# Kernel tuning notes

Hardware: AMD Instinct MI355X
Metric: run time of the kernel (lower is better)

Reference implementation:

```python
import jax, jax.numpy as jnp
import numpy as np

B, C, H, W = 8, 192, 128, 128
CQK = C // 3  # 64


def setup_inputs() -> dict:
    key = jax.random.key(0)
    ks = jax.random.split(key, 8)
    s = 0.05
    return {
        "x": jax.random.normal(ks[0], (B, C, H, W), dtype=jnp.float32),
        "Wq": jax.random.normal(ks[1], (CQK, C), dtype=jnp.float32) * s,
        "bq": jax.random.normal(ks[2], (CQK,), dtype=jnp.float32) * s,
        "Wk": jax.random.normal(ks[3], (CQK, C), dtype=jnp.float32) * s,
        "bk": jax.random.normal(ks[4], (CQK,), dtype=jnp.float32) * s,
        "Wv": jax.random.normal(ks[5], (C, C), dtype=jnp.float32) * s,
        "bv": jax.random.normal(ks[6], (C,), dtype=jnp.float32) * s,
        "gamma": jnp.zeros((1,), dtype=jnp.float32),
    }


def _conv1x1(x, Wt, b):
    # x: [B,C,H,W], Wt: [Cout,Cin] -> [B,Cout,H,W]
    return jnp.einsum('bchw,oc->bohw', x, Wt) + b[None, :, None, None]


def reference(x, Wq, bq, Wk, bk, Wv, bv, gamma):
    Q = _conv1x1(x, Wq, bq)  # [B,CQK,H,W]
    K = _conv1x1(x, Wk, bk)  # [B,CQK,H,W]
    V = _conv1x1(x, Wv, bv)  # [B,C,H,W]

    # Column (vertical) attention logits: query at (h,w) attends to (h2,w)
    e_h = jnp.einsum('bchw,bcgw->bhwg', Q, K)  # [B,H,W,H]
    # mask diagonal h==h2 with -inf (as in MaskAttention)
    diag = jnp.where(jnp.eye(H, dtype=bool), -jnp.inf, 0.0).astype(x.dtype)
    e_h = e_h + diag[:, None, :]  # broadcast over B and W

    # Row (horizontal) attention logits: query at (h,w) attends to (h,w2)
    e_w = jnp.einsum('bchw,bchv->bhwv', Q, K)  # [B,H,W,W]

    # joint softmax over concatenated H+W axis
    att = jax.nn.softmax(jnp.concatenate([e_h, e_w], axis=3), axis=3)
    att_h = att[:, :, :, :H]      # [B,H,W,H]
    att_w = att[:, :, :, H:]      # [B,H,W,W]

    out_h = jnp.einsum('bhwg,bcgw->bchw', att_h, V)
    out_w = jnp.einsum('bhwv,bchv->bchw', att_w, V)
    return gamma * (out_h + out_w) + x
```

## Files before the change

kernel.cpp:

```cpp
#include <hip/hip_runtime.h>
#include <math.h>


#define B_   8
#define C_   192
#define CQK_ 64
#define H_   128
#define W_   128
#define HW_  (H_*W_)

typedef unsigned short u16;
typedef __attribute__((ext_vector_type(8))) short    s16x8;
typedef __attribute__((ext_vector_type(4))) float    f32x4;
typedef __attribute__((ext_vector_type(2))) unsigned u32x2;
#define MFMA_BF16 __builtin_amdgcn_mfma_f32_16x16x32_bf16

__device__ __forceinline__ u16 f2b(float f) {
    unsigned u = __float_as_uint(f);
    return (u16)((u + 0x7fffu + ((u >> 16) & 1u)) >> 16);
}
__device__ __forceinline__ float b2f(u16 v) {
    return __uint_as_float(((unsigned)v) << 16);
}
__device__ __forceinline__ void gll16(const u16* gsrc, unsigned lds_byte) {
    asm volatile("s_mov_b32 m0, %1\n\t"
                 "global_load_lds_dwordx4 %0, off"
                 :: "v"(gsrc), "s"(lds_byte) : "memory");
}

__global__ __launch_bounds__(256) void kwcast(
    const float* __restrict__ Wq, const float* __restrict__ bq,
    const float* __restrict__ Wk, const float* __restrict__ bk,
    const float* __restrict__ Wv, const float* __restrict__ bv,
    u16* __restrict__ Wb, float* __restrict__ Bb)
{
    const int o = blockIdx.x;
    const float *row, *bias; int oo;
    if (o < 64)        { row = Wq; bias = bq; oo = o;       }
    else if (o < 128)  { row = Wk; bias = bk; oo = o - 64;  }
    else               { row = Wv; bias = bv; oo = o - 128; }
    const int t = threadIdx.x;
    if (t < C_) {
        const int p = t >> 6, cc = t & 63;
        Wb[p*20480 + o*64 + (((cc >> 3) ^ (o & 7)) << 3) + (cc & 7)]
            = f2b(row[oo*C_ + t]);
    }
    if (t == C_) Bb[o] = bias[oo];
}

__global__ __launch_bounds__(256) void kxt(
    const float* __restrict__ x, u16* __restrict__ xT)
{
    __shared__ u16 T[24576];
    const int h = blockIdx.x, b = blockIdx.y;
    const float* xb = x + (size_t)b*C_*HW_ + h*W_;
    const int t = threadIdx.x;
    #pragma unroll
    for (int i = 0; i < 24; ++i) {
        const int ridx = i*256 + t;
        const int c = ridx >> 5, wq = (ridx & 31) << 2;
        const f32x4 v = *(const f32x4*)(const void*)(xb + (size_t)c*HW_ + wq);
        u32x2 pk;
        pk.x = (unsigned)f2b(v[0]) | ((unsigned)f2b(v[1]) << 16);
        pk.y = (unsigned)f2b(v[2]) | ((unsigned)f2b(v[3]) << 16);
        *(u32x2*)(void*)&T[c*128 + (((wq >> 3) ^ ((c >> 3) & 15)) << 3) + (wq & 7)] = pk;
    }
    __syncthreads();
    u16* dst = xT + (size_t)(b*H_ + h)*24576;
    #pragma unroll
    for (int i = 0; i < 12; ++i) {
        const int oidx = i*256 + t;
        const int p = oidx >> 10, w = (oidx >> 3) & 127, cp = oidx & 7;
        s16x8 pk;
        #pragma unroll
        for (int e = 0; e < 8; ++e) {
            const int c = p*64 + ((cp ^ (w & 7)) << 3) + e;
            pk[e] = (short)T[c*128 + ((((w >> 3)) ^ ((c >> 3) & 15)) << 3) + (w & 7)];
        }
        *(s16x8*)(void*)(dst + p*8192 + w*64 + cp*8) = pk;
    }
}

__global__ __launch_bounds__(256, 2) void kprojM(
    const u16* __restrict__ xT,
    const u16* __restrict__ Wb, const float* __restrict__ Bb,
    u16* __restrict__ Qc, u16* __restrict__ Kc, u16* __restrict__ Vn)
{
    __shared__ u16 lds[36864];
    u16* ldsW = lds + 16384;
    u16* ldsV = lds + 8192;
    const int h = blockIdx.x, b = blockIdx.y;
    const int t = threadIdx.x, lane = t & 63, wid = t >> 6;
    const int l15 = lane & 15, q = lane >> 4;

    f32x4 acc[8][5];
    #pragma unroll
    for (int ct = 0; ct < 5; ++ct) {
        const float bv = Bb[(ct*4 + wid)*16 + l15];
        #pragma unroll
        for (int r = 0; r < 8; ++r) acc[r][ct] = (f32x4){bv, bv, bv, bv};
    }

    const u16* xTb = xT + (size_t)(b*H_ + h)*24576;
    const unsigned wofs = __builtin_amdgcn_readfirstlane(32768u + (unsigned)wid*1024u);
    const unsigned aofs = __builtin_amdgcn_readfirstlane((unsigned)wid*1024u);

#define STAGE_W(p) do {                                                   \
    const u16* g = Wb + (p)*20480 + wid*512 + lane*8;                     \
    _Pragma("unroll")                                                     \
    for (int i = 0; i < 10; ++i) gll16(g + i*2048, wofs + i*4096); } while(0)
#define STAGE_A(p, ab) do {                                               \
    const u16* g = xTb + (p)*8192 + wid*512 + lane*8;                     \
    _Pragma("unroll")                                                     \
    for (int i = 0; i < 4; ++i)                                           \
        gll16(g + i*2048, aofs + (ab)*16384u + i*4096); } while(0)
#define MFMA_PHASE(ab) do {                                               \
    const u16* bA = lds + (ab)*8192;                                      \
    __builtin_amdgcn_s_setprio(1);                                        \
    _Pragma("unroll")                                                     \
    for (int ks = 0; ks < 2; ++ks) {                                      \
        s16x8 bf[5];                                                      \
        _Pragma("unroll")                                                 \
        for (int ct = 0; ct < 5; ++ct) {                                  \
            const int o = (ct*4 + wid)*16 + l15;                          \
            bf[ct] = *(const s16x8*)(const void*)                         \
                     &ldsW[o*64 + (((ks*4 + q) ^ (o & 7)) << 3)];         \
        }                                                                 \
        _Pragma("unroll")                                                 \
        for (int r = 0; r < 8; ++r) {                                     \
            const int w = r*16 + l15;                                     \
            const s16x8 af = *(const s16x8*)(const void*)                 \
                     &bA[w*64 + (((ks*4 + q) ^ (w & 7)) << 3)];           \
            _Pragma("unroll")                                             \
            for (int ct = 0; ct < 5; ++ct)                                \
                acc[r][ct] = MFMA_BF16(af, bf[ct], acc[r][ct], 0, 0, 0);  \
        }                                                                 \
    }                                                                     \
    __builtin_amdgcn_s_setprio(0); } while(0)

    STAGE_W(0); STAGE_A(0, 0); STAGE_A(1, 1);
    asm volatile("s_waitcnt vmcnt(4)" ::: "memory");
    __builtin_amdgcn_s_barrier();
    MFMA_PHASE(0);
    asm volatile("s_waitcnt lgkmcnt(0)" ::: "memory");
    __builtin_amdgcn_s_barrier();
    STAGE_W(1); STAGE_A(2, 0);
    asm volatile("s_waitcnt vmcnt(4)" ::: "memory");
    __builtin_amdgcn_s_barrier();
    MFMA_PHASE(1);
    asm volatile("s_waitcnt lgkmcnt(0)" ::: "memory");
    __builtin_amdgcn_s_barrier();
    STAGE_W(2);
    asm volatile("s_waitcnt vmcnt(0)" ::: "memory");
    __builtin_amdgcn_s_barrier();
    MFMA_PHASE(0);
    asm volatile("s_waitcnt lgkmcnt(0)" ::: "memory");
    __builtin_amdgcn_s_barrier();

    {
        const int oc = wid*16 + l15;
        #pragma unroll
        for (int r = 0; r < 8; ++r)
            #pragma unroll
            for (int rg = 0; rg < 4; ++rg) {
                const int w = r*16 + q*4 + rg;
                const size_t base = ((size_t)(b*W_ + w)*H_ + h)*CQK_ + oc;
                Qc[base] = f2b(acc[r][0][rg]);
                Kc[base] = f2b(acc[r][1][rg]);
            }
    }
    #pragma unroll
    for (int ct = 2; ct < 5; ++ct) {
        const int c = (ct - 2)*64 + wid*16 + l15;
        #pragma unroll
        for (int r = 0; r < 8; ++r) {
            const int w0 = r*16 + q*4;
            u32x2 pk;
            pk.x = (unsigned)f2b(acc[r][ct][0]) | ((unsigned)f2b(acc[r][ct][1]) << 16);
            pk.y = (unsigned)f2b(acc[r][ct][2]) | ((unsigned)f2b(acc[r][ct][3]) << 16);
            *(u32x2*)(void*)&ldsV[c*128 + (((w0 >> 3) ^ (c & 7)) << 3) + (w0 & 7)] = pk;
        }
    }
    asm volatile("s_waitcnt lgkmcnt(0)" ::: "memory");
    __builtin_amdgcn_s_barrier();
    #pragma unroll
    for (int i = 0; i < 12; ++i) {
        const int idx = i*256 + t;
        const int c = idx >> 4, j = idx & 15;
        const s16x8 v = *(const s16x8*)(const void*)&ldsV[c*128 + j*8];
        *(s16x8*)(void*)&Vn[(size_t)(b*C_ + c)*HW_ + h*W_ + ((j ^ (c & 7)) << 3)] = v;
    }
#undef STAGE_W
#undef STAGE_A
#undef MFMA_PHASE
}

__global__ __launch_bounds__(256) void ktrv(
    const u16* __restrict__ Vn, u16* __restrict__ Vc)
{
    __shared__ u16 T[128*128];
    const int c = blockIdx.x, b = blockIdx.y;
    const u16* src = Vn + (size_t)(b*C_ + c)*HW_;
    u16*       dst = Vc + (size_t)(b*C_ + c)*HW_;
    const int t = threadIdx.x;
    for (int idx = t; idx < 128*16; idx += 256) {
        const int hh = idx >> 4, o = idx & 15;
        s16x8 v = *(const s16x8*)(void*)(src + hh*128 + o*8);
        *(s16x8*)(void*)(T + hh*128 + ((o ^ (hh & 7)) << 3)) = v;
    }
    __syncthreads();
    const int w = t & 127, half = t >> 7;
    for (int seg = 0; seg < 8; ++seg) {
        const int h0 = half*64 + seg*8;
        s16x8 pk;
        #pragma unroll
        for (int k = 0; k < 8; ++k) {
            const int hh = h0 + k;
            const int chunk = (w >> 3) ^ (hh & 7);
            pk[k] = (short)T[hh*128 + (chunk << 3) + (w & 7)];
        }
        *(s16x8*)(void*)(dst + w*128 + h0) = pk;
    }
}

__global__ __launch_bounds__(512) void kC(
    const u16* __restrict__ Qc, const u16* __restrict__ Kc,
    const u16* __restrict__ Vc,
    u16* __restrict__ O2, float* __restrict__ Mh, float* __restrict__ Sh)
{
    extern __shared__ char smem[];
    char* ldsQ = smem;
    char* ldsK = smem + 16384;
    char* ldsP = smem;
    char* ldsV = smem + 32768;
    const int w = blockIdx.x, b = blockIdx.y;
    const int t = threadIdx.x, lane = t & 63, wid = t >> 6;
    const int l15 = lane & 15, q = lane >> 4;

    {
        const u16* qs = Qc + (size_t)(b*W_ + w)*H_*CQK_;
        const u16* ks = Kc + (size_t)(b*W_ + w)*H_*CQK_;
        for (int idx = t; idx < 1024; idx += 512) {
            const int r = idx >> 3, o = idx & 7, so = ((o ^ (r & 7)) << 4);
            *(s16x8*)(ldsQ + r*128 + so) = *(const s16x8*)(void*)(qs + idx*8);
            *(s16x8*)(ldsK + r*128 + so) = *(const s16x8*)(void*)(ks + idx*8);
        }
        for (int idx = t; idx < 3072; idx += 512) {
            const int c = idx >> 4, o = idx & 15;
            s16x8 v = *(const s16x8*)(void*)
                      (Vc + ((size_t)(b*C_ + c)*W_ + w)*H_ + o*8);
            *(s16x8*)(ldsV + c*256 + ((o ^ (c & 7)) << 4)) = v;
        }
    }
    __syncthreads();

    f32x4 accS[8];
    #pragma unroll
    for (int i = 0; i < 8; ++i) accS[i] = (f32x4){0.f,0.f,0.f,0.f};
    const int arow = (wid << 4) + l15;
    #pragma unroll
    for (int ks = 0; ks < 2; ++ks) {
        const int ch = ks*4 + q;
        s16x8 af = *(const s16x8*)(ldsQ + arow*128 + ((ch ^ (arow & 7)) << 4));
        #pragma unroll
        for (int gt = 0; gt < 8; ++gt) {
            const int br = (gt << 4) + l15;
            s16x8 bf = *(const s16x8*)(ldsK + br*128 + ((ch ^ (br & 7)) << 4));
            accS[gt] = MFMA_BF16(af, bf, accS[gt], 0, 0, 0);
        }
    }
    __syncthreads();

    #pragma unroll
    for (int r = 0; r < 4; ++r) {
        const int hh = (wid << 4) + (q << 2) + r;
        #pragma unroll
        for (int gt = 0; gt < 8; ++gt)
            if ((gt << 4) + l15 == hh) accS[gt][r] = -3.0e38f;
        float m = -3.0e38f;
        #pragma unroll
        for (int gt = 0; gt < 8; ++gt) m = fmaxf(m, accS[gt][r]);
        m = fmaxf(m, __shfl_xor(m, 1)); m = fmaxf(m, __shfl_xor(m, 2));
        m = fmaxf(m, __shfl_xor(m, 4)); m = fmaxf(m, __shfl_xor(m, 8));
        float s = 0.f;
        #pragma unroll
        for (int gt = 0; gt < 8; ++gt) {
            const float e = __expf(accS[gt][r] - m);
            s += e;
            const int g = (gt << 4) + l15;
            *(u16*)(ldsP + hh*256 + (((g >> 3) ^ (hh & 7)) << 4) + (g & 7)*2)
                = f2b(e);
        }
        s += __shfl_xor(s, 1); s += __shfl_xor(s, 2);
        s += __shfl_xor(s, 4); s += __shfl_xor(s, 8);
        if (l15 == 0) {
            Mh[(b*W_ + w)*H_ + hh] = m;
            Sh[(b*W_ + w)*H_ + hh] = s;
        }
    }
    __syncthreads();

    f32x4 accO[12];
    #pragma unroll
    for (int i = 0; i < 12; ++i) accO[i] = (f32x4){0.f,0.f,0.f,0.f};
    #pragma unroll
    for (int ks = 0; ks < 4; ++ks) {
        const int ch = ks*4 + q;
        const int pr = (wid << 4) + l15;
        s16x8 af = *(const s16x8*)(ldsP + pr*256 + ((ch ^ (pr & 7)) << 4));
        #pragma unroll
        for (int ct = 0; ct < 12; ++ct) {
            const int vr = (ct << 4) + l15;
            s16x8 bf = *(const s16x8*)(ldsV + vr*256 + ((ch ^ (vr & 7)) << 4));
            accO[ct] = MFMA_BF16(af, bf, accO[ct], 0, 0, 0);
        }
    }
    #pragma unroll
    for (int ct = 0; ct < 12; ++ct) {
        const int c = (ct << 4) + l15;
        #pragma unroll
        for (int r = 0; r < 4; ++r) {
            const int hh = (wid << 4) + (q << 2) + r;
            O2[((size_t)(b*W_ + w)*H_ + hh)*C_ + c] = f2b(accO[ct][r]);
        }
    }
}

__global__ __launch_bounds__(512) void kR(
    const u16* __restrict__ Qc, const u16* __restrict__ Kc,
    const u16* __restrict__ Vn, const u16* __restrict__ O2,
    const float* __restrict__ Mh, const float* __restrict__ Sh,
    const float* __restrict__ x, const float* __restrict__ gamma,
    float* __restrict__ out)
{
    extern __shared__ char smem[];
    char*  ldsQ  = smem;
    char*  ldsK  = smem + 16384;
    char*  ldsP  = smem;
    char*  ldsV  = smem + 32768;
    char*  ldsO2 = smem + 81920;
    float* sMh = (float*)(smem + 133120);
    float* sSh = sMh + 128;
    float* sMw = sSh + 128;
    float* sSw = sMw + 128;
    const int h = blockIdx.x, b = blockIdx.y;
    const int t = threadIdx.x, lane = t & 63, wid = t >> 6;
    const int l15 = lane & 15, q = lane >> 4;
    const float gam = gamma[0];

    for (int idx = t; idx < 1024; idx += 512) {
        const int r = idx >> 3, o = idx & 7, so = ((o ^ (r & 7)) << 4);
        const size_t g = ((size_t)(b*W_ + r)*H_ + h)*CQK_ + o*8;
        *(s16x8*)(ldsQ + r*128 + so) = *(const s16x8*)(void*)(Qc + g);
        *(s16x8*)(ldsK + r*128 + so) = *(const s16x8*)(void*)(Kc + g);
    }
    for (int idx = t; idx < 3072; idx += 512) {
        const int c = idx >> 4, o = idx & 15;
        s16x8 v = *(const s16x8*)(void*)
                  (Vn + (size_t)(b*C_ + c)*HW_ + h*W_ + o*8);
        *(s16x8*)(ldsV + c*256 + ((o ^ (c & 7)) << 4)) = v;
    }
    for (int idx = t; idx < 3200; idx += 512) {
        const int r = idx / 25, o = idx - r*25;
        if (o < 24) {
            s16x8 v = *(const s16x8*)(void*)
                      (O2 + ((size_t)(b*W_ + r)*H_ + h)*C_ + o*8);
            *(s16x8*)(ldsO2 + r*400 + o*16) = v;
        }
    }
    if (t < 128) {
        sMh[t] = Mh[(b*W_ + t)*H_ + h];
        sSh[t] = Sh[(b*W_ + t)*H_ + h];
    }
    __syncthreads();

    f32x4 accS[8];
    #pragma unroll
    for (int i = 0; i < 8; ++i) accS[i] = (f32x4){0.f,0.f,0.f,0.f};
    const int arow = (wid << 4) + l15;
    #pragma unroll
    for (int ks = 0; ks < 2; ++ks) {
        const int ch = ks*4 + q;
        s16x8 af = *(const s16x8*)(ldsQ + arow*128 + ((ch ^ (arow & 7)) << 4));
        #pragma unroll
        for (int vt = 0; vt < 8; ++vt) {
            const int br = (vt << 4) + l15;
            s16x8 bf = *(const s16x8*)(ldsK + br*128 + ((ch ^ (br & 7)) << 4));
            accS[vt] = MFMA_BF16(af, bf, accS[vt], 0, 0, 0);
        }
    }
    __syncthreads();

    #pragma unroll
    for (int r = 0; r < 4; ++r) {
        const int ww = (wid << 4) + (q << 2) + r;
        float m = -3.0e38f;
        #pragma unroll
        for (int vt = 0; vt < 8; ++vt) m = fmaxf(m, accS[vt][r]);
        m = fmaxf(m, __shfl_xor(m, 1)); m = fmaxf(m, __shfl_xor(m, 2));
        m = fmaxf(m, __shfl_xor(m, 4)); m = fmaxf(m, __shfl_xor(m, 8));
        float s = 0.f;
        #pragma unroll
        for (int vt = 0; vt < 8; ++vt) {
            const float e = __expf(accS[vt][r] - m);
            s += e;
            const int v = (vt << 4) + l15;
            *(u16*)(ldsP + ww*256 + (((v >> 3) ^ (ww & 7)) << 4) + (v & 7)*2)
                = f2b(e);
        }
        s += __shfl_xor(s, 1); s += __shfl_xor(s, 2);
        s += __shfl_xor(s, 4); s += __shfl_xor(s, 8);
        if (l15 == 0) { sMw[ww] = m; sSw[ww] = s; }
    }
    __syncthreads();

    f32x4 accO[12];
    #pragma unroll
    for (int i = 0; i < 12; ++i) accO[i] = (f32x4){0.f,0.f,0.f,0.f};
    const int prow = (wid << 4) + l15;
    #pragma unroll
    for (int ks = 0; ks < 4; ++ks) {
        const int ch = ks*4 + q;
        s16x8 bfp = *(const s16x8*)(ldsP + prow*256 + ((ch ^ (prow & 7)) << 4));
        #pragma unroll
        for (int ct = 0; ct < 12; ++ct) {
            const int vr = (ct << 4) + l15;
            s16x8 afv = *(const s16x8*)(ldsV + vr*256 + ((ch ^ (vr & 7)) << 4));
            accO[ct] = MFMA_BF16(afv, bfp, accO[ct], 0, 0, 0);
        }
    }

    const int ww = (wid << 4) + l15;
    const float mh = sMh[ww], shv = sSh[ww];
    const float mw = sMw[ww], swv = sSw[ww];
    const float M  = fmaxf(mh, mw);
    const float S  = shv*__expf(mh - M) + swv*__expf(mw - M);
    const float scw = __expf(mw - M) / S;
    const float sch = __expf(mh - M) / S;
    const size_t gb = (size_t)b*C_*HW_ + h*W_ + ww;
    #pragma unroll
    for (int ct = 0; ct < 12; ++ct) {
        #pragma unroll
        for (int r = 0; r < 4; ++r) {
            const int c = (ct << 4) + (q << 2) + r;
            const float o2 = b2f(*(const u16*)(ldsO2 + ww*400 + c*2));
            const size_t ga = gb + (size_t)c*HW_;
            out[ga] = gam*(accO[ct][r]*scw + o2*sch) + x[ga];
        }
    }
}

extern "C" void kernel_launch(void* const* d_in, const int* in_sizes, int n_in,
                              void* d_out, int out_size, void* d_ws, size_t ws_size,
                              hipStream_t stream)
{
    const float* x  = (const float*)d_in[0];
    const float* Wq = (const float*)d_in[1];
    const float* bq = (const float*)d_in[2];
    const float* Wk = (const float*)d_in[3];
    const float* bk = (const float*)d_in[4];
    const float* Wv = (const float*)d_in[5];
    const float* bv = (const float*)d_in[6];
    const float* gm = (const float*)d_in[7];
    float* out = (float*)d_out;

    u16* Qc = (u16*)d_ws;
    u16* Kc = Qc + 8388608;
    u16* Vn = Kc + 8388608;
    u16* Vc = Vn + 25165824;
    u16* O2 = Vc + 25165824;
    u16* xT = O2;
    float* Mh = (float*)(O2 + 25165824);
    float* Sh = Mh + 131072;
    u16*  Wb = (u16*)(Sh + 131072);
    float* Bb = (float*)(Wb + 61440);

    hipLaunchKernelGGL(kwcast, dim3(320), dim3(256), 0, stream,
                       Wq, bq, Wk, bk, Wv, bv, Wb, Bb);
    hipLaunchKernelGGL(kxt, dim3(H_, B_), dim3(256), 0, stream, x, xT);
    hipLaunchKernelGGL(kprojM, dim3(H_, B_), dim3(256), 0, stream,
                       xT, Wb, Bb, Qc, Kc, Vn);
    hipLaunchKernelGGL(ktrv, dim3(C_, B_), dim3(256), 0, stream, Vn, Vc);
    hipLaunchKernelGGL(kC, dim3(W_, B_), dim3(512), 81920, stream,
                       Qc, Kc, Vc, O2, Mh, Sh);
    hipLaunchKernelGGL(kR, dim3(H_, B_), dim3(512), 135168, stream,
                       Qc, Kc, Vn, O2, Mh, Sh, x, gm, out);
}
```

Baseline: 204.1 us.

## Split row-attention V product into two channel halves to shrink LDS footprint

```diff
diff --git a/kernel.cpp b/kernel.cpp
--- a/kernel.cpp
+++ b/kernel.cpp
@@ -321,12 +321,12 @@
         #pragma unroll
         for (int r = 0; r < 4; ++r) {
             const int hh = (wid << 4) + (q << 2) + r;
-            O2[((size_t)(b*W_ + w)*H_ + hh)*C_ + c] = f2b(accO[ct][r]);
-        }
-    }
-}
-
-__global__ __launch_bounds__(512) void kR(
+            O2[((size_t)(b*H_ + hh)*W_ + w)*C_ + c] = f2b(accO[ct][r]);
+        }
+    }
+}
+
+__global__ __launch_bounds__(512, 4) void kR(
     const u16* __restrict__ Qc, const u16* __restrict__ Kc,
     const u16* __restrict__ Vn, const u16* __restrict__ O2,
     const float* __restrict__ Mh, const float* __restrict__ Sh,
@@ -334,12 +334,11 @@
     float* __restrict__ out)
 {
     extern __shared__ char smem[];
-    char*  ldsQ  = smem;
-    char*  ldsK  = smem + 16384;
-    char*  ldsP  = smem;
-    char*  ldsV  = smem + 32768;
-    char*  ldsO2 = smem + 81920;
-    float* sMh = (float*)(smem + 133120);
+    char*  ldsQ = smem;
+    char*  ldsK = smem + 16384;
+    char*  ldsP = smem;
+    char*  ldsV = smem + 32768;
+    float* sMh = (float*)(smem + 57344);
     float* sSh = sMh + 128;
     float* sMw = sSh + 128;
     float* sSw = sMw + 128;
@@ -348,25 +347,24 @@
     const int l15 = lane & 15, q = lane >> 4;
     const float gam = gamma[0];
 
+    s16x8 vh2[3];
+    #pragma unroll
+    for (int i = 0; i < 3; ++i) {
+        const int idx = i*512 + t;
+        const int c = 96 + (idx >> 4), o = idx & 15;
+        vh2[i] = *(const s16x8*)(void*)(Vn + (size_t)(b*C_ + c)*HW_ + h*W_ + o*8);
+    }
     for (int idx = t; idx < 1024; idx += 512) {
         const int r = idx >> 3, o = idx & 7, so = ((o ^ (r & 7)) << 4);
         const size_t g = ((size_t)(b*W_ + r)*H_ + h)*CQK_ + o*8;
         *(s16x8*)(ldsQ + r*128 + so) = *(const s16x8*)(void*)(Qc + g);
         *(s16x8*)(ldsK + r*128 + so) = *(const s16x8*)(void*)(Kc + g);
     }
-    for (int idx = t; idx < 3072; idx += 512) {
+    for (int idx = t; idx < 1536; idx += 512) {
         const int c = idx >> 4, o = idx & 15;
         s16x8 v = *(const s16x8*)(void*)
                   (Vn + (size_t)(b*C_ + c)*HW_ + h*W_ + o*8);
         *(s16x8*)(ldsV + c*256 + ((o ^ (c & 7)) << 4)) = v;
-    }
-    for (int idx = t; idx < 3200; idx += 512) {
-        const int r = idx / 25, o = idx - r*25;
-        if (o < 24) {
-            s16x8 v = *(const s16x8*)(void*)
-                      (O2 + ((size_t)(b*W_ + r)*H_ + h)*C_ + o*8);
-            *(s16x8*)(ldsO2 + r*400 + o*16) = v;
-        }
     }
     if (t < 128) {
         sMh[t] = Mh[(b*W_ + t)*H_ + h];
@@ -414,20 +412,28 @@
     }
     __syncthreads();
 
-    f32x4 accO[12];
-    #pragma unroll
-    for (int i = 0; i < 12; ++i) accO[i] = (f32x4){0.f,0.f,0.f,0.f};
     const int prow = (wid << 4) + l15;
+    f32x4 accO[6];
+    #pragma unroll
+    for (int i = 0; i < 6; ++i) accO[i] = (f32x4){0.f,0.f,0.f,0.f};
     #pragma unroll
     for (int ks = 0; ks < 4; ++ks) {
         const int ch = ks*4 + q;
         s16x8 bfp = *(const s16x8*)(ldsP + prow*256 + ((ch ^ (prow & 7)) << 4));
         #pragma unroll
-        for (int ct = 0; ct < 12; ++ct) {
+        for (int ct = 0; ct < 6; ++ct) {
             const int vr = (ct << 4) + l15;
             s16x8 afv = *(const s16x8*)(ldsV + vr*256 + ((ch ^ (vr & 7)) << 4));
             accO[ct] = MFMA_BF16(afv, bfp, accO[ct], 0, 0, 0);
         }
+    }
+    __syncthreads();
+
+    #pragma unroll
+    for (int i = 0; i < 3; ++i) {
+        const int idx = i*512 + t;
+        const int lc = idx >> 4, o = idx & 15;
+        *(s16x8*)(ldsV + lc*256 + ((o ^ ((lc + 96) & 7)) << 4)) = vh2[i];
     }
 
     const int ww = (wid << 4) + l15;
@@ -437,15 +443,43 @@
     const float S  = shv*__expf(mh - M) + swv*__expf(mw - M);
     const float scw = __expf(mw - M) / S;
     const float sch = __expf(mh - M) / S;
+    const u16* o2p = O2 + ((size_t)(b*H_ + h)*W_ + ww)*C_;
     const size_t gb = (size_t)b*C_*HW_ + h*W_ + ww;
-    #pragma unroll
-    for (int ct = 0; ct < 12; ++ct) {
+
+    #pragma unroll
+    for (int ct = 0; ct < 6; ++ct) {
         #pragma unroll
         for (int r = 0; r < 4; ++r) {
-            const int c = (ct << 4) + (q << 2) + r;
-            const float o2 = b2f(*(const u16*)(ldsO2 + ww*400 + c*2));
+            const int c = ct*16 + q*4 + r;
+            const float o2 = b2f(o2p[c]);
             const size_t ga = gb + (size_t)c*HW_;
             out[ga] = gam*(accO[ct][r]*scw + o2*sch) + x[ga];
+        }
+    }
+    __syncthreads();
+
+    f32x4 accO2[6];
+    #pragma unroll
+    for (int i = 0; i < 6; ++i) accO2[i] = (f32x4){0.f,0.f,0.f,0.f};
+    #pragma unroll
+    for (int ks = 0; ks < 4; ++ks) {
+        const int ch = ks*4 + q;
+        s16x8 bfp = *(const s16x8*)(ldsP + prow*256 + ((ch ^ (prow & 7)) << 4));
+        #pragma unroll
+        for (int ct = 0; ct < 6; ++ct) {
+            const int lr = (ct << 4) + l15;
+            s16x8 afv = *(const s16x8*)(ldsV + lr*256 + ((ch ^ ((lr + 96) & 7)) << 4));
+            accO2[ct] = MFMA_BF16(afv, bfp, accO2[ct], 0, 0, 0);
+        }
+    }
+    #pragma unroll
+    for (int ct = 0; ct < 6; ++ct) {
+        #pragma unroll
+        for (int r = 0; r < 4; ++r) {
+            const int c = 96 + ct*16 + q*4 + r;
+            const float o2 = b2f(o2p[c]);
+            const size_t ga = gb + (size_t)c*HW_;
+            out[ga] = gam*(accO2[ct][r]*scw + o2*sch) + x[ga];
         }
     }
 }
@@ -483,6 +517,6 @@
     hipLaunchKernelGGL(ktrv, dim3(C_, B_), dim3(256), 0, stream, Vn, Vc);
     hipLaunchKernelGGL(kC, dim3(W_, B_), dim3(512), 81920, stream,
                        Qc, Kc, Vc, O2, Mh, Sh);
-    hipLaunchKernelGGL(kR, dim3(H_, B_), dim3(512), 135168, stream,
+    hipLaunchKernelGGL(kR, dim3(H_, B_), dim3(512), 59392, stream,
                        Qc, Kc, Vn, O2, Mh, Sh, x, gm, out);
 }
```

Result: slower. 219.8 us (+7.7%).

## Shrink LDS in attention kernels by staging V in chunks and register-resident Q

Applied to the files above, without the earlier changes.

```diff
diff --git a/kernel.cpp b/kernel.cpp
--- a/kernel.cpp
+++ b/kernel.cpp
@@ -223,45 +223,54 @@
     }
 }
 
-__global__ __launch_bounds__(512) void kC(
+__global__ __launch_bounds__(512, 6) void kC(
     const u16* __restrict__ Qc, const u16* __restrict__ Kc,
     const u16* __restrict__ Vc,
     u16* __restrict__ O2, float* __restrict__ Mh, float* __restrict__ Sh)
 {
     extern __shared__ char smem[];
-    char* ldsQ = smem;
-    char* ldsK = smem + 16384;
+    char* ldsK = smem;
     char* ldsP = smem;
     char* ldsV = smem + 32768;
     const int w = blockIdx.x, b = blockIdx.y;
     const int t = threadIdx.x, lane = t & 63, wid = t >> 6;
     const int l15 = lane & 15, q = lane >> 4;
-
+    const int arow = (wid << 4) + l15;
+
+    const u16* qrow = Qc + ((size_t)(b*W_ + w)*H_ + arow)*CQK_;
+    s16x8 qf0 = *(const s16x8*)(const void*)(qrow + q*8);
+    s16x8 qf1 = *(const s16x8*)(const void*)(qrow + (4 + q)*8);
+    s16x8 vh[2];
+    #pragma unroll
+    for (int i = 0; i < 2; ++i) {
+        const int idx = i*512 + t;
+        const int c = 64 + (idx >> 4), o = idx & 15;
+        vh[i] = *(const s16x8*)(const void*)
+                (Vc + ((size_t)(b*C_ + c)*W_ + w)*H_ + o*8);
+    }
     {
-        const u16* qs = Qc + (size_t)(b*W_ + w)*H_*CQK_;
-        const u16* ks = Kc + (size_t)(b*W_ + w)*H_*CQK_;
+        const u16* ksrc = Kc + (size_t)(b*W_ + w)*H_*CQK_;
         for (int idx = t; idx < 1024; idx += 512) {
-            const int r = idx >> 3, o = idx & 7, so = ((o ^ (r & 7)) << 4);
-            *(s16x8*)(ldsQ + r*128 + so) = *(const s16x8*)(void*)(qs + idx*8);
-            *(s16x8*)(ldsK + r*128 + so) = *(const s16x8*)(void*)(ks + idx*8);
-        }
-        for (int idx = t; idx < 3072; idx += 512) {
-            const int c = idx >> 4, o = idx & 15;
-            s16x8 v = *(const s16x8*)(void*)
-                      (Vc + ((size_t)(b*C_ + c)*W_ + w)*H_ + o*8);
-            *(s16x8*)(ldsV + c*256 + ((o ^ (c & 7)) << 4)) = v;
-        }
+            const int r = idx >> 3, o = idx & 7;
+            *(s16x8*)(ldsK + r*128 + ((o ^ (r & 7)) << 4)) =
+                *(const s16x8*)(const void*)(ksrc + idx*8);
+        }
+    }
+    for (int idx = t; idx < 1024; idx += 512) {
+        const int lc = idx >> 4, o = idx & 15;
+        *(s16x8*)(ldsV + lc*256 + ((o ^ (lc & 7)) << 4)) =
+            *(const s16x8*)(const void*)
+            (Vc + ((size_t)(b*C_ + lc)*W_ + w)*H_ + o*8);
     }
     __syncthreads();
 
     f32x4 accS[8];
     #pragma unroll
     for (int i = 0; i < 8; ++i) accS[i] = (f32x4){0.f,0.f,0.f,0.f};
-    const int arow = (wid << 4) + l15;
     #pragma unroll
     for (int ks = 0; ks < 2; ++ks) {
         const int ch = ks*4 + q;
-        s16x8 af = *(const s16x8*)(ldsQ + arow*128 + ((ch ^ (arow & 7)) << 4));
+        const s16x8 af = ks ? qf1 : qf0;
         #pragma unroll
         for (int gt = 0; gt < 8; ++gt) {
             const int br = (gt << 4) + l15;
@@ -298,35 +307,71 @@
             Sh[(b*W_ + w)*H_ + hh] = s;
         }
     }
-    __syncthreads();
-
-    f32x4 accO[12];
-    #pragma unroll
-    for (int i = 0; i < 12; ++i) accO[i] = (f32x4){0.f,0.f,0.f,0.f};
-    #pragma unroll
-    for (int ks = 0; ks < 4; ++ks) {
-        const int ch = ks*4 + q;
-        const int pr = (wid << 4) + l15;
-        s16x8 af = *(const s16x8*)(ldsP + pr*256 + ((ch ^ (pr & 7)) << 4));
-        #pragma unroll
-        for (int ct = 0; ct < 12; ++ct) {
-            const int vr = (ct << 4) + l15;
-            s16x8 bf = *(const s16x8*)(ldsV + vr*256 + ((ch ^ (vr & 7)) << 4));
-            accO[ct] = MFMA_BF16(af, bf, accO[ct], 0, 0, 0);
-        }
-    }
-    #pragma unroll
-    for (int ct = 0; ct < 12; ++ct) {
-        const int c = (ct << 4) + l15;
-        #pragma unroll
-        for (int r = 0; r < 4; ++r) {
-            const int hh = (wid << 4) + (q << 2) + r;
-            O2[((size_t)(b*W_ + w)*H_ + hh)*C_ + c] = f2b(accO[ct][r]);
-        }
-    }
-}
-
-__global__ __launch_bounds__(512) void kR(
+
+#define KC_PV(accv) do {                                                  \
+    _Pragma("unroll")                                                     \
+    for (int ks = 0; ks < 4; ++ks) {                                      \
+        const int ch = ks*4 + q;                                          \
+        s16x8 afp = *(const s16x8*)(ldsP + arow*256 + ((ch ^ (arow & 7)) << 4)); \
+        _Pragma("unroll")                                                 \
+        for (int ct = 0; ct < 4; ++ct) {                                  \
+            const int vr = (ct << 4) + l15;                               \
+            s16x8 bfv = *(const s16x8*)(ldsV + vr*256 + ((ch ^ (vr & 7)) << 4)); \
+            accv[ct] = MFMA_BF16(afp, bfv, accv[ct], 0, 0, 0);            \
+        }                                                                 \
+    } } while(0)
+#define KC_O2W(accv, cb) do {                                             \
+    _Pragma("unroll")                                                     \
+    for (int ct = 0; ct < 4; ++ct) {                                      \
+        const int c = (cb) + (ct << 4) + l15;                             \
+        _Pragma("unroll")                                                 \
+        for (int r = 0; r < 4; ++r) {                                     \
+            const int hh = (wid << 4) + (q << 2) + r;                     \
+            O2[((size_t)(b*H_ + hh)*W_ + w)*C_ + c] = f2b(accv[ct][r]);   \
+        }                                                                 \
+    } } while(0)
+
+    f32x4 accO[4];
+    #pragma unroll
+    for (int i = 0; i < 4; ++i) accO[i] = (f32x4){0.f,0.f,0.f,0.f};
+    KC_PV(accO);
+    __syncthreads();
+    #pragma unroll
+    for (int i = 0; i < 2; ++i) {
+        const int idx = i*512 + t;
+        const int lc = idx >> 4, o = idx & 15;
+        *(s16x8*)(ldsV + lc*256 + ((o ^ (lc & 7)) << 4)) = vh[i];
+    }
+    #pragma unroll
+    for (int i = 0; i < 2; ++i) {
+        const int idx = i*512 + t;
+        const int c = 128 + (idx >> 4), o = idx & 15;
+        vh[i] = *(const s16x8*)(const void*)
+                (Vc + ((size_t)(b*C_ + c)*W_ + w)*H_ + o*8);
+    }
+    __syncthreads();
+    KC_O2W(accO, 0);
+    #pragma unroll
+    for (int i = 0; i < 4; ++i) accO[i] = (f32x4){0.f,0.f,0.f,0.f};
+    KC_PV(accO);
+    __syncthreads();
+    #pragma unroll
+    for (int i = 0; i < 2; ++i) {
+        const int idx = i*512 + t;
+        const int lc = idx >> 4, o = idx & 15;
+        *(s16x8*)(ldsV + lc*256 + ((o ^ (lc & 7)) << 4)) = vh[i];
+    }
+    __syncthreads();
+    KC_O2W(accO, 64);
+    #pragma unroll
+    for (int i = 0; i < 4; ++i) accO[i] = (f32x4){0.f,0.f,0.f,0.f};
+    KC_PV(accO);
+    KC_O2W(accO, 128);
+#undef KC_PV
+#undef KC_O2W
+}
+
+__global__ __launch_bounds__(512, 6) void kR(
     const u16* __restrict__ Qc, const u16* __restrict__ Kc,
     const u16* __restrict__ Vn, const u16* __restrict__ O2,
     const float* __restrict__ Mh, const float* __restrict__ Sh,
@@ -334,54 +379,50 @@
     float* __restrict__ out)
 {
     extern __shared__ char smem[];
-    char*  ldsQ  = smem;
-    char*  ldsK  = smem + 16384;
+    char*  ldsK  = smem;
     char*  ldsP  = smem;
     char*  ldsV  = smem + 32768;
-    char*  ldsO2 = smem + 81920;
-    float* sMh = (float*)(smem + 133120);
-    float* sSh = sMh + 128;
-    float* sMw = sSh + 128;
-    float* sSw = sMw + 128;
+    float* sScw  = (float*)(smem + 49152);
+    float* sSch  = (float*)(smem + 49664);
     const int h = blockIdx.x, b = blockIdx.y;
     const int t = threadIdx.x, lane = t & 63, wid = t >> 6;
     const int l15 = lane & 15, q = lane >> 4;
+    const int arow = (wid << 4) + l15;
+    const int wbase = (wid << 4) + (q << 2);
     const float gam = gamma[0];
 
+    const u16* qrow = Qc + ((size_t)(b*W_ + arow)*H_ + h)*CQK_;
+    s16x8 qf0 = *(const s16x8*)(const void*)(qrow + q*8);
+    s16x8 qf1 = *(const s16x8*)(const void*)(qrow + (4 + q)*8);
+    s16x8 vh[2];
+    #pragma unroll
+    for (int i = 0; i < 2; ++i) {
+        const int idx = i*512 + t;
+        const int c = 64 + (idx >> 4), o = idx & 15;
+        vh[i] = *(const s16x8*)(const void*)
+                (Vn + (size_t)(b*C_ + c)*HW_ + h*W_ + o*8);
+    }
     for (int idx = t; idx < 1024; idx += 512) {
-        const int r = idx >> 3, o = idx & 7, so = ((o ^ (r & 7)) << 4);
-        const size_t g = ((size_t)(b*W_ + r)*H_ + h)*CQK_ + o*8;
-        *(s16x8*)(ldsQ + r*128 + so) = *(const s16x8*)(void*)(Qc + g);
-        *(s16x8*)(ldsK + r*128 + so) = *(const s16x8*)(void*)(Kc + g);
-    }
-    for (int idx = t; idx < 3072; idx += 512) {
-        const int c = idx >> 4, o = idx & 15;
-        s16x8 v = *(const s16x8*)(void*)
-                  (Vn + (size_t)(b*C_ + c)*HW_ + h*W_ + o*8);
-        *(s16x8*)(ldsV + c*256 + ((o ^ (c & 7)) << 4)) = v;
-    }
-    for (int idx = t; idx < 3200; idx += 512) {
-        const int r = idx / 25, o = idx - r*25;
-        if (o < 24) {
-            s16x8 v = *(const s16x8*)(void*)
-                      (O2 + ((size_t)(b*W_ + r)*H_ + h)*C_ + o*8);
-            *(s16x8*)(ldsO2 + r*400 + o*16) = v;
-        }
-    }
-    if (t < 128) {
-        sMh[t] = Mh[(b*W_ + t)*H_ + h];
-        sSh[t] = Sh[(b*W_ + t)*H_ + h];
+        const int r = idx >> 3, o = idx & 7;
+        *(s16x8*)(ldsK + r*128 + ((o ^ (r & 7)) << 4)) =
+            *(const s16x8*)(const void*)
+            (Kc + ((size_t)(b*W_ + r)*H_ + h)*CQK_ + o*8);
+    }
+    for (int idx = t; idx < 1024; idx += 512) {
+        const int lc = idx >> 4, o = idx & 15;
+        *(s16x8*)(ldsV + lc*256 + ((o ^ (lc & 7)) << 4)) =
+            *(const s16x8*)(const void*)
+            (Vn + (size_t)(b*C_ + lc)*HW_ + h*W_ + o*8);
     }
     __syncthreads();
 
     f32x4 accS[8];
     #pragma unroll
     for (int i = 0; i < 8; ++i) accS[i] = (f32x4){0.f,0.f,0.f,0.f};
-    const int arow = (wid << 4) + l15;
     #pragma unroll
     for (int ks = 0; ks < 2; ++ks) {
         const int ch = ks*4 + q;
-        s16x8 af = *(const s16x8*)(ldsQ + arow*128 + ((ch ^ (arow & 7)) << 4));
+        const s16x8 af = ks ? qf1 : qf0;
         #pragma unroll
         for (int vt = 0; vt < 8; ++vt) {
             const int br = (vt << 4) + l15;
@@ -410,44 +451,99 @@
         }
         s += __shfl_xor(s, 1); s += __shfl_xor(s, 2);
         s += __shfl_xor(s, 4); s += __shfl_xor(s, 8);
-        if (l15 == 0) { sMw[ww] = m; sSw[ww] = s; }
-    }
-    __syncthreads();
-
-    f32x4 accO[12];
-    #pragma unroll
-    for (int i = 0; i < 12; ++i) accO[i] = (f32x4){0.f,0.f,0.f,0.f};
-    const int prow = (wid << 4) + l15;
-    #pragma unroll
-    for (int ks = 0; ks < 4; ++ks) {
-        const int ch = ks*4 + q;
-        s16x8 bfp = *(const s16x8*)(ldsP + prow*256 + ((ch ^ (prow & 7)) << 4));
-        #pragma unroll
-        for (int ct = 0; ct < 12; ++ct) {
-            const int vr = (ct << 4) + l15;
-            s16x8 afv = *(const s16x8*)(ldsV + vr*256 + ((ch ^ (vr & 7)) << 4));
-            accO[ct] = MFMA_BF16(afv, bfp, accO[ct], 0, 0, 0);
-        }
-    }
-
-    const int ww = (wid << 4) + l15;
-    const float mh = sMh[ww], shv = sSh[ww];
-    const float mw = sMw[ww], swv = sSw[ww];
-    const float M  = fmaxf(mh, mw);
-    const float S  = shv*__expf(mh - M) + swv*__expf(mw - M);
-    const float scw = __expf(mw - M) / S;
-    const float sch = __expf(mh - M) / S;
-    const size_t gb = (size_t)b*C_*HW_ + h*W_ + ww;
-    #pragma unroll
-    for (int ct = 0; ct < 12; ++ct) {
-        #pragma unroll
-        for (int r = 0; r < 4; ++r) {
-            const int c = (ct << 4) + (q << 2) + r;
-            const float o2 = b2f(*(const u16*)(ldsO2 + ww*400 + c*2));
-            const size_t ga = gb + (size_t)c*HW_;
-            out[ga] = gam*(accO[ct][r]*scw + o2*sch) + x[ga];
-        }
-    }
+        if (l15 == 0) {
+            const float mh  = Mh[(b*W_ + ww)*H_ + h];
+            const float shv = Sh[(b*W_ + ww)*H_ + h];
+            const float M = fmaxf(mh, m);
+            const float S = shv*__expf(mh - M) + s*__expf(m - M);
+            sScw[ww] = __expf(m - M) / S;
+            sSch[ww] = __expf(mh - M) / S;
+        }
+    }
+
+    const u16* o2p = O2 + (size_t)(b*H_ + h)*W_*C_;
+    float scw[4], sch[4];
+    #pragma unroll
+    for (int r = 0; r < 4; ++r) { scw[r] = sScw[wbase + r]; sch[r] = sSch[wbase + r]; }
+
+#define KR_PV(accv) do {                                                  \
+    _Pragma("unroll")                                                     \
+    for (int ks = 0; ks < 4; ++ks) {                                      \
+        const int ch = ks*4 + q;                                          \
+        s16x8 afp = *(const s16x8*)(ldsP + arow*256 + ((ch ^ (arow & 7)) << 4)); \
+        _Pragma("unroll")                                                 \
+        for (int ct = 0; ct < 4; ++ct) {                                  \
+            const int vr = (ct << 4) + l15;                               \
+            s16x8 bfv = *(const s16x8*)(ldsV + vr*256 + ((ch ^ (vr & 7)) << 4)); \
+            accv[ct] = MFMA_BF16(afp, bfv, accv[ct], 0, 0, 0);            \
+        }                                                                 \
+    } } while(0)
+#define KR_PREF(k, o2k, xk) do {                                          \
+    _Pragma("unroll")                                                     \
+    for (int ct = 0; ct < 4; ++ct) {                                      \
+        const int c = (k)*64 + (ct << 4) + l15;                           \
+        _Pragma("unroll")                                                 \
+        for (int r = 0; r < 4; ++r)                                       \
+            o2k[ct][r] = o2p[(size_t)(wbase + r)*C_ + c];                 \
+        xk[ct] = *(const f32x4*)(const void*)                             \
+                 (x + (size_t)(b*C_ + c)*HW_ + h*W_ + wbase);             \
+    } } while(0)
+#define KR_EPI(k, accv, o2k, xk) do {                                     \
+    _Pragma("unroll")                                                     \
+    for (int ct = 0; ct < 4; ++ct) {                                      \
+        const int c = (k)*64 + (ct << 4) + l15;                           \
+        f32x4 res;                                                        \
+        _Pragma("unroll")                                                 \
+        for (int r = 0; r < 4; ++r)                                       \
+            res[r] = gam*(accv[ct][r]*scw[r] + b2f(o2k[ct][r])*sch[r]) + xk[ct][r]; \
+        *(f32x4*)(void*)(out + (size_t)(b*C_ + c)*HW_ + h*W_ + wbase) = res; \
+    } } while(0)
+
+    u16  o2a[4][4]; f32x4 xpa[4];
+    KR_PREF(0, o2a, xpa);
+    f32x4 accO[4];
+    #pragma unroll
+    for (int i = 0; i < 4; ++i) accO[i] = (f32x4){0.f,0.f,0.f,0.f};
+    KR_PV(accO);
+    __syncthreads();
+    #pragma unroll
+    for (int i = 0; i < 2; ++i) {
+        const int idx = i*512 + t;
+        const int lc = idx >> 4, o = idx & 15;
+        *(s16x8*)(ldsV + lc*256 + ((o ^ (lc & 7)) << 4)) = vh[i];
+    }
+    #pragma unroll
+    for (int i = 0; i < 2; ++i) {
+        const int idx = i*512 + t;
+        const int c = 128 + (idx >> 4), o = idx & 15;
+        vh[i] = *(const s16x8*)(const void*)
+                (Vn + (size_t)(b*C_ + c)*HW_ + h*W_ + o*8);
+    }
+    u16  o2b[4][4]; f32x4 xpb[4];
+    KR_PREF(1, o2b, xpb);
+    __syncthreads();
+    KR_EPI(0, accO, o2a, xpa);
+    #pragma unroll
+    for (int i = 0; i < 4; ++i) accO[i] = (f32x4){0.f,0.f,0.f,0.f};
+    KR_PV(accO);
+    __syncthreads();
+    #pragma unroll
+    for (int i = 0; i < 2; ++i) {
+        const int idx = i*512 + t;
+        const int lc = idx >> 4, o = idx & 15;
+        *(s16x8*)(ldsV + lc*256 + ((o ^ (lc & 7)) << 4)) = vh[i];
+    }
+    u16  o2c[4][4]; f32x4 xpc[4];
+    KR_PREF(2, o2c, xpc);
+    __syncthreads();
+    KR_EPI(1, accO, o2b, xpb);
+    #pragma unroll
+    for (int i = 0; i < 4; ++i) accO[i] = (f32x4){0.f,0.f,0.f,0.f};
+    KR_PV(accO);
+    KR_EPI(2, accO, o2c, xpc);
+#undef KR_PV
+#undef KR_PREF
+#undef KR_EPI
 }
 
 extern "C" void kernel_launch(void* const* d_in, const int* in_sizes, int n_in,
@@ -481,8 +577,8 @@
     hipLaunchKernelGGL(kprojM, dim3(H_, B_), dim3(256), 0, stream,
                        xT, Wb, Bb, Qc, Kc, Vn);
     hipLaunchKernelGGL(ktrv, dim3(C_, B_), dim3(256), 0, stream, Vn, Vc);
-    hipLaunchKernelGGL(kC, dim3(W_, B_), dim3(512), 81920, stream,
+    hipLaunchKernelGGL(kC, dim3(W_, B_), dim3(512), 49152, stream,
                        Qc, Kc, Vc, O2, Mh, Sh);
-    hipLaunchKernelGGL(kR, dim3(H_, B_), dim3(512), 135168, stream,
+    hipLaunchKernelGGL(kR, dim3(H_, B_), dim3(512), 50176, stream,
                        Qc, Kc, Vn, O2, Mh, Sh, x, gm, out);
 }
```

Measured after the change: 259.8 us. +27.3%, slower.
